# Performance work log

Measured on AMD Instinct MI355X. Metric: run time of the kernel, lower is better.

Reference implementation:

```python
import jax, jax.numpy as jnp
import numpy as np

EPS = 1e-6  # clamp epsilon in GeM
NORM_EPS = 1e-12  # torch F.normalize eps
PATCH_SIZES = (3,)


def l2norm(x, axis):
    n = jnp.sqrt(jnp.sum(x * x, axis=axis, keepdims=True))
    return x / jnp.maximum(n, NORM_EPS)


def setup_inputs() -> dict:
    key = jax.random.key(0)
    k1, k2, k3 = jax.random.split(key, 3)
    N, D, H, W, F = 16, 2048, 32, 32, 512
    x = jax.random.normal(k1, (N, D, H, W), jnp.float32)
    proj_w = jax.random.normal(k2, (F, D), jnp.float32) * (1.0 / np.sqrt(D))
    proj_b = jax.random.normal(k3, (F,), jnp.float32) * 0.01
    p = jnp.full((1,), 3.0, jnp.float32)
    return {"x": x, "proj_w": proj_w, "proj_b": proj_b, "p": p}


def reference(x, proj_w, proj_b, p):
    # ---- GeM global descriptor (global_pool path inside local_pool) ----
    x = l2norm(x, axis=1)                                  # L2 over channel dim
    g = jnp.clip(x, EPS, None) ** p[0]                     # [N,D,H,W]
    g = g.mean(axis=(-2, -1))                              # [N,D]
    g = g ** (1.0 / p[0])
    g = g @ proj_w.T + proj_b                              # [N,F]
    g = l2norm(g, axis=1)

    # ---- integral image over spatial dims ----
    integ = jnp.cumsum(jnp.cumsum(x, axis=-1), axis=-2)    # [N,D,H,W]

    local_descs = []
    for ps in PATCH_SIZES:
        off = ps // 2
        # zero-pad (1+off) on top/left, then replicate-pad off on bottom/right
        ipad = jnp.pad(integ, ((0, 0), (0, 0), (1 + off, 0), (1 + off, 0)))
        ipad = jnp.pad(ipad, ((0, 0), (0, 0), (0, off), (0, off)), mode='edge')
        # box sum via 4-corner integral-image difference
        # == grouped 2x2 conv with dilation=ps, weights [[1,-1],[-1,1]], stride=1
        box = (ipad[:, :, :-ps, :-ps] - ipad[:, :, :-ps, ps:]
               - ipad[:, :, ps:, :-ps] + ipad[:, :, ps:, ps:])  # [N,D,H,W]
        N, D, Hh, Ww = box.shape
        pd = box.reshape(N, D, Hh * Ww).transpose(0, 2, 1)  # [N,HW,D]
        pd = pd @ proj_w.T + proj_b                         # [N,HW,F]
        pd = l2norm(pd, axis=2)
        local_descs.append(pd.transpose(0, 2, 1))           # [N,F,HW]

    return g, local_descs[0]
```

## Files before the change

kernel.cpp:

```cpp
#include <hip/hip_runtime.h>
#include <hip/hip_bf16.h>

#define N_ 16
#define D_ 2048
#define H_ 32
#define W_ 32
#define HW_ 1024
#define F_ 512

typedef unsigned short u16;
typedef unsigned int u32;
typedef __attribute__((ext_vector_type(8))) short bf16x8;
typedef __attribute__((ext_vector_type(4))) float f32x4;

__device__ __forceinline__ u16 f2bf(float f) {
  union { float fv; u32 u; } c; c.fv = f;
  u32 u = c.u;
  u32 r = (u + 0x7fffu + ((u >> 16) & 1u)) >> 16;
  return (u16)r;
}

#define GLD_LDS16(gp, lp) __builtin_amdgcn_global_load_lds( \
    (const __attribute__((address_space(1))) void*)(gp), \
    (__attribute__((address_space(3))) void*)(lp), 16, 0, 0)

__global__ __launch_bounds__(256) void k_zero(float* __restrict__ p) {
  int i = blockIdx.x * 256 + threadIdx.x;
  ((float4*)p)[i] = (float4){0.f, 0.f, 0.f, 0.f};
}

__global__ __launch_bounds__(256) void k_sumsq(const float* __restrict__ x, float* __restrict__ sumsq) {
  const int n = blockIdx.x;
  const int dc = blockIdx.y;
  const int t = threadIdx.x;
  const float* xp = x + ((size_t)n * D_ + (size_t)dc * 64) * HW_;
  float s0 = 0.f, s1 = 0.f, s2 = 0.f, s3 = 0.f;
  for (int d = 0; d < 64; ++d) {
    const float* row = xp + (size_t)d * HW_;
    float v0 = row[t], v1 = row[t + 256], v2 = row[t + 512], v3 = row[t + 768];
    s0 += v0 * v0; s1 += v1 * v1; s2 += v2 * v2; s3 += v3 * v3;
  }
  atomicAdd(&sumsq[n * HW_ + t      ], s0);
  atomicAdd(&sumsq[n * HW_ + t + 256], s1);
  atomicAdd(&sumsq[n * HW_ + t + 512], s2);
  atomicAdd(&sumsq[n * HW_ + t + 768], s3);
}

__global__ __launch_bounds__(256) void k_box2(const float* __restrict__ x,
    const float* __restrict__ sumsq, const float* __restrict__ pvec,
    float* __restrict__ gbuf, u16* __restrict__ packA) {
  const int n = blockIdx.x, ht = blockIdx.y, dc = blockIdx.z;
  const int h0 = ht * 4, d0 = dc * 64;
  const int t = threadIdx.x;
  const int w4 = t & 7, dg = t >> 3;
  const int wq = w4 * 4;
  const float p = pvec[0];
  const bool p3 = (p == 3.0f);

  __shared__ __align__(16) u16 sbox[128 * 68];
  __shared__ __align__(16) float rnl[6][32];

  if (t < 192) {
    int jj = t >> 5, w = t & 31;
    int hp = h0 - 1 + jj;
    float r = 0.f;
    if (hp >= 0 && hp < H_) r = 1.0f / fmaxf(sqrtf(sumsq[n * HW_ + hp * W_ + w]), 1e-12f);
    rnl[jj][w] = r;
  }
  __syncthreads();

  float s0 = 0.f, s1 = 0.f;
  #pragma unroll
  for (int dj = 0; dj < 2; ++dj) {
    const int d = d0 + dg * 2 + dj;
    const float* base = x + ((size_t)(n * D_ + d)) * HW_ + wq;
    float4 v[6];
    #pragma unroll
    for (int jj = 0; jj < 6; ++jj) {
      int hp = h0 - 1 + jj;
      if (hp >= 0 && hp < H_) {
        float4 xv = *(const float4*)(base + hp * W_);
        float4 rr = *(const float4*)(&rnl[jj][wq]);
        v[jj].x = xv.x * rr.x; v[jj].y = xv.y * rr.y;
        v[jj].z = xv.z * rr.z; v[jj].w = xv.w * rr.w;
      } else {
        v[jj] = (float4){0.f, 0.f, 0.f, 0.f};
      }
    }
    float g = 0.f;
    #pragma unroll
    for (int jj = 1; jj <= 4; ++jj) {
      float cx = fmaxf(v[jj].x, 1e-6f), cy = fmaxf(v[jj].y, 1e-6f);
      float cz = fmaxf(v[jj].z, 1e-6f), cw = fmaxf(v[jj].w, 1e-6f);
      if (p3) g += cx * cx * cx + cy * cy * cy + cz * cz * cz + cw * cw * cw;
      else    g += __powf(cx, p) + __powf(cy, p) + __powf(cz, p) + __powf(cw, p);
    }
    if (dj == 0) s0 = g; else s1 = g;
    #pragma unroll
    for (int jj = 0; jj < 6; ++jj) {
      float lf = __shfl_up(v[jj].w, 1, 8);
      float rf = __shfl_down(v[jj].x, 1, 8);
      if (w4 == 0) lf = 0.f;
      if (w4 == 7) rf = 0.f;
      float4 h;
      h.x = lf + v[jj].x + v[jj].y;
      h.y = v[jj].x + v[jj].y + v[jj].z;
      h.z = v[jj].y + v[jj].z + v[jj].w;
      h.w = v[jj].z + v[jj].w + rf;
      v[jj] = h;
    }
    #pragma unroll
    for (int k = 0; k < 4; ++k) {
      float4 b;
      b.x = v[k].x + v[k + 1].x + v[k + 2].x;
      b.y = v[k].y + v[k + 1].y + v[k + 2].y;
      b.z = v[k].z + v[k + 1].z + v[k + 2].z;
      b.w = v[k].w + v[k + 1].w + v[k + 2].w;
      const int rb = k * 32 + wq;
      sbox[(rb + 0) * 68 + dg * 2 + dj] = f2bf(b.x);
      sbox[(rb + 1) * 68 + dg * 2 + dj] = f2bf(b.y);
      sbox[(rb + 2) * 68 + dg * 2 + dj] = f2bf(b.z);
      sbox[(rb + 3) * 68 + dg * 2 + dj] = f2bf(b.w);
    }
  }
  __syncthreads();

  {
    const int r = t >> 1, half = t & 1;
    const u16* srcp = sbox + r * 68 + half * 32;
    uint2 a[8];
    #pragma unroll
    for (int q = 0; q < 8; ++q) a[q] = *(const uint2*)(srcp + q * 4);
    const int mt = n * 16 + ht * 2 + (r >> 6);
    const int mf = (r >> 4) & 3, r15 = r & 15;
    const int kt = dc * 2 + half;
    u16* dst = packA + ((size_t)(mt * 64 + kt) * 4 + mf) * 512 + r15 * 8;
    #pragma unroll
    for (int q = 0; q < 4; ++q) {
      uint4 b;
      b.x = a[2 * q].x; b.y = a[2 * q].y; b.z = a[2 * q + 1].x; b.w = a[2 * q + 1].y;
      *(uint4*)(dst + q * 128) = b;
    }
  }

  {
    float v0 = s0, v1 = s1;
    v0 += __shfl_xor(v0, 1, 8); v1 += __shfl_xor(v1, 1, 8);
    v0 += __shfl_xor(v0, 2, 8); v1 += __shfl_xor(v1, 2, 8);
    v0 += __shfl_xor(v0, 4, 8); v1 += __shfl_xor(v1, 4, 8);
    if (w4 == 0) {
      atomicAdd(&gbuf[n * D_ + d0 + dg * 2    ], v0);
      atomicAdd(&gbuf[n * D_ + d0 + dg * 2 + 1], v1);
    }
  }
}

__global__ __launch_bounds__(256) void k_wconv(const float* __restrict__ w, u16* __restrict__ packB) {
  const int i = blockIdx.x * 256 + threadIdx.x;
  const int lane = i & 63, nf = (i >> 6) & 3, kt = (i >> 8) & 63, wq = i >> 14;
  const int r15 = lane & 15, hi = lane >> 4;
  const int f = wq * 64 + nf * 16 + r15;
  const int k = kt * 32 + hi * 8;
  const float* src = w + (size_t)f * D_ + k;
  float4 v0 = *(const float4*)(src);
  float4 v1 = *(const float4*)(src + 4);
  u16 r[8] = { f2bf(v0.x), f2bf(v0.y), f2bf(v0.z), f2bf(v0.w),
               f2bf(v1.x), f2bf(v1.y), f2bf(v1.z), f2bf(v1.w) };
  *(uint4*)(packB + (size_t)i * 8) = *(const uint4*)r;
}

__global__ __launch_bounds__(512) void k_gemm(const u16* __restrict__ packA,
    const u16* __restrict__ packB, const float* __restrict__ bias,
    float* __restrict__ outL) {
  const int n  = blockIdx.x >> 4;
  const int mtl = blockIdx.x & 15;
  const int mt = blockIdx.x;
  const int hw0 = mtl * 64;
  const int t = threadIdx.x;
  const int lane = t & 63, wv = t >> 6;
  const int r15 = lane & 15, hi = lane >> 4;

  __shared__ __align__(16) float smem_f[128 * 68];
  __shared__ float s_sq[8][64];
  __shared__ float s_rn[64];

  f32x4 acc[4][4];
  #pragma unroll
  for (int a = 0; a < 4; ++a)
    #pragma unroll
    for (int b = 0; b < 4; ++b) acc[a][b] = (f32x4){0.f, 0.f, 0.f, 0.f};

  const u16* asrc = packA + ((size_t)(mt * 64) * 4 + (wv & 3)) * 512 + lane * 8;
  const u16* bbase = packB + (size_t)wv * 131072 + lane * 8;

#define STAGE_A(KT) GLD_LDS16(asrc + (size_t)(KT) * 2048, \
    (char*)smem_f + ((KT) & 3) * 4096 + (wv & 3) * 1024)

  STAGE_A(0);
  STAGE_A(1);
  bf16x8 bc[4], bn[4];
  #pragma unroll
  for (int nf = 0; nf < 4; ++nf) bc[nf] = *(const bf16x8*)(bbase + nf * 512);

  for (int kt = 0; kt < 64; ++kt) {
    if (kt + 2 < 64) STAGE_A(kt + 2);
    if (kt + 1 < 64) {
      #pragma unroll
      for (int nf = 0; nf < 4; ++nf)
        bn[nf] = *(const bf16x8*)(bbase + ((kt + 1) * 4 + nf) * 512);
    }
    __builtin_amdgcn_sched_barrier(0);
    if (kt < 62) {
      asm volatile("s_waitcnt vmcnt(5)" ::: "memory");
    } else if (kt == 62) {
      asm volatile("s_waitcnt vmcnt(4)" ::: "memory");
    } else {
      asm volatile("s_waitcnt vmcnt(0)" ::: "memory");
    }
    __builtin_amdgcn_sched_barrier(0);
    __builtin_amdgcn_s_barrier();
    __builtin_amdgcn_sched_barrier(0);

    const u16* sA = (const u16*)((const char*)smem_f + (kt & 3) * 4096);
    bf16x8 af[4];
    #pragma unroll
    for (int mf = 0; mf < 4; ++mf)
      af[mf] = *(const bf16x8*)(sA + mf * 512 + lane * 8);
    #pragma unroll
    for (int mf = 0; mf < 4; ++mf)
      #pragma unroll
      for (int nf = 0; nf < 4; ++nf)
        acc[mf][nf] = __builtin_amdgcn_mfma_f32_16x16x32_bf16(af[mf], bc[nf], acc[mf][nf], 0, 0, 0);
    #pragma unroll
    for (int nf = 0; nf < 4; ++nf) bc[nf] = bn[nf];
  }
#undef STAGE_A

  float badd[4];
  #pragma unroll
  for (int nf = 0; nf < 4; ++nf) badd[nf] = bias[wv * 64 + nf * 16 + r15];
  #pragma unroll
  for (int mf = 0; mf < 4; ++mf)
    #pragma unroll
    for (int nf = 0; nf < 4; ++nf)
      #pragma unroll
      for (int j = 0; j < 4; ++j) acc[mf][nf][j] += badd[nf];

  #pragma unroll
  for (int mf = 0; mf < 4; ++mf)
    #pragma unroll
    for (int j = 0; j < 4; ++j) {
      float s = 0.f;
      #pragma unroll
      for (int nf = 0; nf < 4; ++nf) { float v = acc[mf][nf][j]; s += v * v; }
      s += __shfl_xor(s, 1); s += __shfl_xor(s, 2); s += __shfl_xor(s, 4); s += __shfl_xor(s, 8);
      if ((lane & 15) == 0) s_sq[wv][mf * 16 + hi * 4 + j] = s;
    }
  __syncthreads();
  if (t < 64) {
    float s = 0.f;
    #pragma unroll
    for (int w8 = 0; w8 < 8; ++w8) s += s_sq[w8][t];
    s_rn[t] = 1.0f / fmaxf(sqrtf(s), 1e-12f);
  }
  __syncthreads();

  float* ct = smem_f;
  for (int nf = 0; nf < 4; ++nf) {
    const int fi = wv * 16 + r15;
    #pragma unroll
    for (int mf = 0; mf < 4; ++mf)
      #pragma unroll
      for (int j = 0; j < 4; ++j) {
        int m = mf * 16 + hi * 4 + j;
        ct[fi * 68 + m] = acc[mf][nf][j] * s_rn[m];
      }
    __syncthreads();
    {
      int fr = t >> 2, mq = t & 3;
      int f = (fr >> 4) * 64 + nf * 16 + (fr & 15);
      float* dst = outL + ((size_t)(n * F_ + f)) * HW_ + hw0 + mq * 16;
      const float* srcp = ct + fr * 68 + mq * 16;
      float4 a0 = *(const float4*)(srcp);
      float4 a1 = *(const float4*)(srcp + 4);
      float4 a2 = *(const float4*)(srcp + 8);
      float4 a3 = *(const float4*)(srcp + 12);
      *(float4*)(dst) = a0; *(float4*)(dst + 4) = a1;
      *(float4*)(dst + 8) = a2; *(float4*)(dst + 12) = a3;
    }
    __syncthreads();
  }
}

__global__ __launch_bounds__(256) void k_gem_fin(const float* __restrict__ gbuf,
    const float* __restrict__ pvec, float* __restrict__ gg) {
  int i = blockIdx.x * 256 + threadIdx.x;
  float p = pvec[0];
  float m = gbuf[i] * (1.0f / 1024.0f);
  gg[i] = (p == 3.0f) ? cbrtf(m) : powf(m, 1.0f / p);
}

__global__ __launch_bounds__(256) void k_gproj(const float* __restrict__ w,
    const float* __restrict__ bias, const float* __restrict__ gg,
    float* __restrict__ gproj) {
  const int f = blockIdx.x;
  const int t = threadIdx.x;
  float wreg[8];
  #pragma unroll
  for (int j = 0; j < 8; ++j) wreg[j] = w[(size_t)f * D_ + t + j * 256];
  __shared__ float red[4];
  const int lane = t & 63, wv = t >> 6;
  for (int n = 0; n < N_; ++n) {
    float s = 0.f;
    #pragma unroll
    for (int j = 0; j < 8; ++j) s += wreg[j] * gg[n * D_ + t + j * 256];
    #pragma unroll
    for (int off = 32; off >= 1; off >>= 1) s += __shfl_down(s, off);
    if (lane == 0) red[wv] = s;
    __syncthreads();
    if (t == 0) gproj[n * F_ + f] = red[0] + red[1] + red[2] + red[3] + bias[f];
    __syncthreads();
  }
}

__global__ __launch_bounds__(512) void k_gnorm(const float* __restrict__ gproj, float* __restrict__ outg) {
  const int n = blockIdx.x;
  const int t = threadIdx.x;
  float v = gproj[n * F_ + t];
  float s = v * v;
  const int lane = t & 63, wv = t >> 6;
  #pragma unroll
  for (int off = 32; off >= 1; off >>= 1) s += __shfl_down(s, off);
  __shared__ float red[8];
  __shared__ float rtot;
  if (lane == 0) red[wv] = s;
  __syncthreads();
  if (t == 0) {
    float a = 0.f;
    #pragma unroll
    for (int i = 0; i < 8; ++i) a += red[i];
    rtot = 1.0f / fmaxf(sqrtf(a), 1e-12f);
  }
  __syncthreads();
  outg[n * F_ + t] = v * rtot;
}

extern "C" void kernel_launch(void* const* d_in, const int* in_sizes, int n_in,
                              void* d_out, int out_size, void* d_ws, size_t ws_size,
                              hipStream_t stream) {
  const float* x  = (const float*)d_in[0];
  const float* pw = (const float*)d_in[1];
  const float* pb = (const float*)d_in[2];
  const float* pv = (const float*)d_in[3];
  float* out = (float*)d_out;

  char* ws = (char*)d_ws;
  float* sumsq = (float*)ws;
  float* gbuf  = (float*)(ws + 65536);
  float* gg    = (float*)(ws + 65536 + 131072);
  float* gproj = (float*)(ws + 65536 + 2 * 131072);
  u16*   packB = (u16*)(ws + 65536 + 2 * 131072 + 32768);
  u16*   packA = (u16*)(ws + 4u * 1024u * 1024u);

  k_zero<<<dim3(48), dim3(256), 0, stream>>>(sumsq);
  k_sumsq<<<dim3(16, 32), dim3(256), 0, stream>>>(x, sumsq);
  k_wconv<<<dim3(512), dim3(256), 0, stream>>>(pw, packB);
  k_box2<<<dim3(16, 8, 32), dim3(256), 0, stream>>>(x, sumsq, pv, gbuf, packA);
  k_gem_fin<<<dim3(128), dim3(256), 0, stream>>>(gbuf, pv, gg);
  k_gproj<<<dim3(512), dim3(256), 0, stream>>>(pw, pb, gg, gproj);
  k_gnorm<<<dim3(16), dim3(512), 0, stream>>>(gproj, out);
  k_gemm<<<dim3(256), dim3(512), 0, stream>>>(packA, packB, pb, out + N_ * F_);
}
```

Before: 139.7 us.

## Process two K-tiles per iteration with deeper A staging ring and MFMA priority

Restructures the projection GEMM main loop to handle two K-steps per iteration. It widens the LDS ring for A from 4 to 8 slots, prefetches B for two steps ahead, and issues the A stages after the barrier. MFMA issue is wrapped in s_setprio to favour matrix work. The aim is to halve the barrier and waitcnt overhead per K-step and to keep more loads in flight, at the cost of more registers and LDS.

```diff
diff --git a/kernel.cpp b/kernel.cpp
--- a/kernel.cpp
+++ b/kernel.cpp
@@ -194,45 +194,61 @@
   const u16* bbase = packB + (size_t)wv * 131072 + lane * 8;
 
 #define STAGE_A(KT) GLD_LDS16(asrc + (size_t)(KT) * 2048, \
-    (char*)smem_f + ((KT) & 3) * 4096 + (wv & 3) * 1024)
-
-  STAGE_A(0);
-  STAGE_A(1);
-  bf16x8 bc[4], bn[4];
-  #pragma unroll
-  for (int nf = 0; nf < 4; ++nf) bc[nf] = *(const bf16x8*)(bbase + nf * 512);
-
-  for (int kt = 0; kt < 64; ++kt) {
-    if (kt + 2 < 64) STAGE_A(kt + 2);
-    if (kt + 1 < 64) {
+    (char*)smem_f + ((KT) & 7) * 4096 + (wv & 3) * 1024)
+
+  bf16x8 bc[4], bc2[4], bn[4], bn2[4];
+  #pragma unroll
+  for (int nf = 0; nf < 4; ++nf) bc[nf]  = *(const bf16x8*)(bbase + nf * 512);
+  #pragma unroll
+  for (int nf = 0; nf < 4; ++nf) bc2[nf] = *(const bf16x8*)(bbase + (4 + nf) * 512);
+  __builtin_amdgcn_sched_barrier(0);
+  #pragma unroll
+  for (int q = 0; q < 4; ++q) STAGE_A(q);
+  __builtin_amdgcn_sched_barrier(0);
+
+  for (int i = 0; i < 32; ++i) {
+    if (i + 1 < 32) {
       #pragma unroll
       for (int nf = 0; nf < 4; ++nf)
-        bn[nf] = *(const bf16x8*)(bbase + ((kt + 1) * 4 + nf) * 512);
+        bn[nf]  = *(const bf16x8*)(bbase + ((2 * i + 2) * 4 + nf) * 512);
+      #pragma unroll
+      for (int nf = 0; nf < 4; ++nf)
+        bn2[nf] = *(const bf16x8*)(bbase + ((2 * i + 3) * 4 + nf) * 512);
     }
     __builtin_amdgcn_sched_barrier(0);
-    if (kt < 62) {
-      asm volatile("s_waitcnt vmcnt(5)" ::: "memory");
-    } else if (kt == 62) {
-      asm volatile("s_waitcnt vmcnt(4)" ::: "memory");
+    if (i < 31) {
+      asm volatile("s_waitcnt vmcnt(10)" ::: "memory");
     } else {
       asm volatile("s_waitcnt vmcnt(0)" ::: "memory");
     }
     __builtin_amdgcn_sched_barrier(0);
     __builtin_amdgcn_s_barrier();
     __builtin_amdgcn_sched_barrier(0);
-
-    const u16* sA = (const u16*)((const char*)smem_f + (kt & 3) * 4096);
-    bf16x8 af[4];
+    if (i <= 29) { STAGE_A(2 * i + 4); STAGE_A(2 * i + 5); }
+    __builtin_amdgcn_sched_barrier(0);
+
+    const u16* sA0 = (const u16*)((const char*)smem_f + ((2 * i) & 7) * 4096);
+    const u16* sA1 = (const u16*)((const char*)smem_f + ((2 * i + 1) & 7) * 4096);
+    bf16x8 af0[4], af1[4];
+    #pragma unroll
+    for (int mf = 0; mf < 4; ++mf) {
+      af0[mf] = *(const bf16x8*)(sA0 + mf * 512 + lane * 8);
+      af1[mf] = *(const bf16x8*)(sA1 + mf * 512 + lane * 8);
+    }
+    __builtin_amdgcn_s_setprio(1);
     #pragma unroll
     for (int mf = 0; mf < 4; ++mf)
-      af[mf] = *(const bf16x8*)(sA + mf * 512 + lane * 8);
+      #pragma unroll
+      for (int nf = 0; nf < 4; ++nf)
+        acc[mf][nf] = __builtin_amdgcn_mfma_f32_16x16x32_bf16(af0[mf], bc[nf], acc[mf][nf], 0, 0, 0);
     #pragma unroll
     for (int mf = 0; mf < 4; ++mf)
       #pragma unroll
       for (int nf = 0; nf < 4; ++nf)
-        acc[mf][nf] = __builtin_amdgcn_mfma_f32_16x16x32_bf16(af[mf], bc[nf], acc[mf][nf], 0, 0, 0);
-    #pragma unroll
-    for (int nf = 0; nf < 4; ++nf) bc[nf] = bn[nf];
+        acc[mf][nf] = __builtin_amdgcn_mfma_f32_16x16x32_bf16(af1[mf], bc2[nf], acc[mf][nf], 0, 0, 0);
+    __builtin_amdgcn_s_setprio(0);
+    #pragma unroll
+    for (int nf = 0; nf < 4; ++nf) { bc[nf] = bn[nf]; bc2[nf] = bn2[nf]; }
   }
 #undef STAGE_A
 
```

Measured after the change: 144.2 us. 1.03x slower.
